# Optimization experiments

Hardware: AMD Instinct MI355X
Metric: run time of the kernel (lower is better)

Reference implementation:

```python
import jax, jax.numpy as jnp
import numpy as np

GROUPS = 32
EPS = 1e-5


def group_norm(x, gamma, beta):
    # x: [B, C, H, W]; normalize over (C//G, H, W) within each of G groups
    B, C, H, W = x.shape
    xg = x.reshape(B, GROUPS, C // GROUPS, H, W)
    mean = xg.mean(axis=(2, 3, 4), keepdims=True)
    var = xg.var(axis=(2, 3, 4), keepdims=True)
    xg = (xg - mean) * jax.lax.rsqrt(var + EPS)
    x = xg.reshape(B, C, H, W)
    return x * gamma[None, :, None, None] + beta[None, :, None, None]


def conv1x1(x, W, b):
    # 1x1 conv == pointwise linear over channels. x: [B,C,H,W], W: [Cout,Cin]
    return jnp.einsum('oc,bchw->bohw', W, x) + b[None, :, None, None]


def setup_inputs() -> dict:
    key = jax.random.key(0)
    ks = jax.random.split(key, 6)
    B, C, H, W = 16, 512, 32, 32
    scale = 1.0 / np.sqrt(C)  # ~kaiming-ish init for 1x1 convs
    return {
        'x': jax.random.normal(ks[0], (B, C, H, W), jnp.float32),
        'gn_gamma': jnp.ones((C,), jnp.float32),
        'gn_beta': jnp.zeros((C,), jnp.float32),
        'Wq': jax.random.normal(ks[1], (C, C), jnp.float32) * scale,
        'bq': jnp.zeros((C,), jnp.float32),
        'Wk': jax.random.normal(ks[2], (C, C), jnp.float32) * scale,
        'bk': jnp.zeros((C,), jnp.float32),
        'Wv': jax.random.normal(ks[3], (C, C), jnp.float32) * scale,
        'bv': jnp.zeros((C,), jnp.float32),
        'Wp': jax.random.normal(ks[4], (C, C), jnp.float32) * scale,
        'bp': jnp.zeros((C,), jnp.float32),
    }


def reference(x, gn_gamma, gn_beta, Wq, bq, Wk, bk, Wv, bv, Wp, bp):
    B, C, H, W = x.shape
    h = group_norm(x, gn_gamma, gn_beta)
    q = conv1x1(h, Wq, bq).reshape(B, C, H * W)  # [B,C,T]
    k = conv1x1(h, Wk, bk).reshape(B, C, H * W)
    v = conv1x1(h, Wv, bv).reshape(B, C, H * W)
    # scores [B, T(query), S(key)] = q^T k, scaled by C^{-1/2}
    w = jnp.einsum('bct,bcs->bts', q, k) * (C ** -0.5)
    w = jax.nn.softmax(w, axis=-1)
    h = jnp.einsum('bts,bcs->bct', w, v).reshape(B, C, H, W)
    h = conv1x1(h, Wp, bp)
    return x + h
```

## Files before the change

kernel.cpp:

```cpp
#include <hip/hip_runtime.h>

typedef unsigned short u16;
typedef __bf16 bf16x8 __attribute__((ext_vector_type(8)));
typedef float f32x4 __attribute__((ext_vector_type(4)));

__device__ __forceinline__ u16 f2bf(float f) {
    unsigned u = __builtin_bit_cast(unsigned, f);
    u += 0x7fffu + ((u >> 16) & 1u);
    return (u16)(u >> 16);
}
__device__ __forceinline__ float bf2f(u16 h) {
    return __builtin_bit_cast(float, (unsigned)h << 16);
}

#define GLDS16(g, l) __builtin_amdgcn_global_load_lds( \
    (const __attribute__((address_space(1))) void*)(g), \
    (__attribute__((address_space(3))) void*)(l), 16, 0, 0)

#define QK_SCALE 0.044194173824159216f

__global__ __launch_bounds__(256) void fused_pre(
    const float* __restrict__ Wq, const float* __restrict__ Wk,
    const float* __restrict__ Wv, const float* __restrict__ Wp,
    const float* __restrict__ bq, const float* __restrict__ bk,
    const float* __restrict__ bv,
    u16* __restrict__ Wqkv, u16* __restrict__ Wpb, float* __restrict__ bqkv,
    float* __restrict__ rsum,
    const float* __restrict__ x, float2* __restrict__ stats)
{
    __shared__ float rs[4], rs2[4];
    const int tid = threadIdx.x;

    if (blockIdx.x < 4096) {
        int idx = blockIdx.x * 256 + tid;
        if (idx < 786432) {
            int which = idx >> 18;
            int off   = idx & 262143;
            if (which == 0)
                Wqkv[idx] = f2bf(Wq[off] * QK_SCALE);
            else
                Wqkv[idx] = f2bf(((which == 1) ? Wk : Wv)[off]);
        } else {
            int off = idx - 786432;
            Wpb[off] = f2bf(Wp[off]);
        }
        if (idx < 1536) {
            float bvv = (idx < 512) ? bq[idx] * QK_SCALE
                      : (idx < 1024) ? bk[idx & 511] : bv[idx & 511];
            bqkv[idx] = bvv;
        }
        if (idx < 16384) rsum[idx] = 0.f;
        return;
    }

    const int rem = blockIdx.x - 4096;
    const int g = rem & 31, b = rem >> 5;
    const float* xg = x + ((size_t)b * 512 + (size_t)g * 16) * 1024;

    float s = 0.f, s2 = 0.f;
    const float4* x4 = (const float4*)xg;
    #pragma unroll 4
    for (int i = tid; i < 4096; i += 256) {
        float4 v = x4[i];
        s  += v.x + v.y + v.z + v.w;
        s2 += v.x * v.x + v.y * v.y + v.z * v.z + v.w * v.w;
    }
    #pragma unroll
    for (int off = 32; off; off >>= 1) {
        s  += __shfl_down(s, off);
        s2 += __shfl_down(s2, off);
    }
    const int w = tid >> 6;
    if ((tid & 63) == 0) { rs[w] = s; rs2[w] = s2; }
    __syncthreads();
    if (tid == 0) {
        float S  = rs[0] + rs[1] + rs[2] + rs[3];
        float S2 = rs2[0] + rs2[1] + rs2[2] + rs2[3];
        float mean = S * (1.f / 16384.f);
        float var  = S2 * (1.f / 16384.f) - mean * mean;
        stats[b * 32 + g] = make_float2(mean, rsqrtf(var + 1e-5f));
    }
}

__global__ __launch_bounds__(256) void gn_apply(
    const float* __restrict__ x, const float* __restrict__ gamma,
    const float* __restrict__ beta, const float2* __restrict__ stats,
    u16* __restrict__ ht)
{
    const int tc = blockIdx.x, b = blockIdx.y, tid = threadIdx.x;
    const int t0 = tc * 32;

    __shared__ float2 st[32];
    __shared__ float ga[512], be[512];
    __shared__ __align__(16) u16 tile[512 * 32];

    if (tid < 32) st[tid] = stats[b * 32 + tid];
    for (int c = tid; c < 512; c += 256) { ga[c] = gamma[c]; be[c] = beta[c]; }
    __syncthreads();

    #pragma unroll
    for (int pass = 0; pass < 16; pass++) {
        const int c = pass * 32 + (tid >> 3);
        const int f = tid & 7;
        float4 v = *(const float4*)(x + ((size_t)(b * 512 + c)) * 1024 + t0 + f * 4);
        float2 s = st[c >> 4];
        float sc = s.y * ga[c];
        float sh = be[c] - s.x * sc;
        ushort4 hv = {f2bf(v.x * sc + sh), f2bf(v.y * sc + sh),
                      f2bf(v.z * sc + sh), f2bf(v.w * sc + sh)};
        const int slot = f ^ (c & 7) ^ ((c >> 3) & 7);
        *(ushort4*)(tile + c * 32 + slot * 4) = hv;
    }
    __syncthreads();

    #pragma unroll
    for (int p = 0; p < 8; p++) {
        const int t = p * 4 + (tid >> 6);
        const int l = tid & 63;
        u16 tmp[8];
        #pragma unroll
        for (int e = 0; e < 8; e++) {
            const int c = l * 8 + e;
            const int slot = (t >> 2) ^ (c & 7) ^ ((c >> 3) & 7);
            tmp[e] = tile[c * 32 + slot * 4 + (t & 3)];
        }
        *(uint4*)(ht + ((size_t)b * 1024 + t0 + t) * 512 + l * 8) = *(uint4*)tmp;
    }
}

template <int MODE>
__global__ __launch_bounds__(512, 2) void gemm_big(
    const u16* __restrict__ A, const u16* __restrict__ B,
    size_t strideA, size_t strideB, int lda, int ldb, int K,
    u16* __restrict__ o0, u16* __restrict__ o1, u16* __restrict__ o2,
    const float* __restrict__ bias)
{
    __shared__ __align__(16) u16 smem[73728];
    u16* As = smem;
    u16* Bs = smem + 49152;

    const int tid  = threadIdx.x;
    const int lane = tid & 63;
    const int wave = tid >> 6;
    const int wm   = (wave & 3) * 64;
    const int wn   = (wave >> 2) * 64;

    const int gx = gridDim.x, gy = gridDim.y;
    int f = blockIdx.x + gx * (blockIdx.y + gy * blockIdx.z);
    const int nwg = gx * gy * (int)gridDim.z;
    f = (f & 7) * (nwg >> 3) + (f >> 3);
    const int bx  = f % gx;
    const int byz = f / gx;
    const int by  = byz % gy;
    const int b   = byz / gy;

    const u16* Ab = A + (size_t)b * strideA + (size_t)by * 256 * lda;
    const u16* Bb = B + (size_t)b * strideB + (size_t)bx * 128 * ldb;

    const int srow = tid >> 3;
    const int sc   = tid & 7;
    const int scg  = sc ^ (srow & 7);

    const u16* aSrc[4]; int aDst[4];
    #pragma unroll
    for (int u = 0; u < 4; u++) {
        aSrc[u] = Ab + (size_t)(u * 64 + srow) * lda + scg * 8;
        aDst[u] = (u * 64 + srow) * 64 + sc * 8;
    }
    const u16* bSrc[2]; int bDst[2];
    #pragma unroll
    for (int u = 0; u < 2; u++) {
        bSrc[u] = Bb + (size_t)(u * 64 + srow) * ldb + scg * 8;
        bDst[u] = (u * 64 + srow) * 64 + sc * 8;
    }

    const int l15 = lane & 15, lh = lane >> 4, rx = lane & 7;
    int aOff[4][2], bOff[4][2];
    #pragma unroll
    for (int i = 0; i < 4; i++)
        #pragma unroll
        for (int ks = 0; ks < 2; ks++) {
            const int slot = ((ks << 2) + lh) ^ rx;
            aOff[i][ks] = (wm + i * 16 + l15) * 64 + slot * 8;
            bOff[i][ks] = (wn + i * 16 + l15) * 64 + slot * 8;
        }

    f32x4 acc[4][4] = {};
    const int NT = K >> 6;

    #pragma unroll
    for (int u = 0; u < 4; u++) GLDS16(aSrc[u], As + aDst[u]);
    #pragma unroll
    for (int u = 0; u < 2; u++) GLDS16(bSrc[u], Bs + bDst[u]);
    #pragma unroll
    for (int u = 0; u < 4; u++) GLDS16(aSrc[u] + 64, As + 16384 + aDst[u]);
    #pragma unroll
    for (int u = 0; u < 2; u++) GLDS16(bSrc[u] + 64, Bs + 8192 + bDst[u]);

    int cbuf = 0, sbuf = 2;
    for (int t = 0; t < NT; ++t) {
        if (t == NT - 1) asm volatile("s_waitcnt vmcnt(0)" ::: "memory");
        else             asm volatile("s_waitcnt vmcnt(6)" ::: "memory");
        __builtin_amdgcn_s_barrier();

        const u16* Ac = As + cbuf * 16384;
        const u16* Bc = Bs + cbuf * 8192;
        u16* Asb = As + sbuf * 16384;
        u16* Bsb = Bs + sbuf * 8192;
        const int ko = (t + 2) * 64;
        const bool pf = (t + 2 < NT);

        if (pf) {
            GLDS16(aSrc[0] + ko, Asb + aDst[0]);
            GLDS16(aSrc[1] + ko, Asb + aDst[1]);
            GLDS16(bSrc[0] + ko, Bsb + bDst[0]);
        }
        {
            bf16x8 af[4], bfr[4];
            #pragma unroll
            for (int i = 0; i < 4; i++) {
                af[i]  = *(const bf16x8*)(Ac + aOff[i][0]);
                bfr[i] = *(const bf16x8*)(Bc + bOff[i][0]);
            }
            __builtin_amdgcn_s_setprio(1);
            #pragma unroll
            for (int mi = 0; mi < 4; mi++)
                #pragma unroll
                for (int nj = 0; nj < 4; nj++)
                    acc[mi][nj] = __builtin_amdgcn_mfma_f32_16x16x32_bf16(
                        af[mi], bfr[nj], acc[mi][nj], 0, 0, 0);
            __builtin_amdgcn_s_setprio(0);
        }
        if (pf) {
            GLDS16(aSrc[2] + ko, Asb + aDst[2]);
            GLDS16(aSrc[3] + ko, Asb + aDst[3]);
            GLDS16(bSrc[1] + ko, Bsb + bDst[1]);
        }
        {
            bf16x8 af[4], bfr[4];
            #pragma unroll
            for (int i = 0; i < 4; i++) {
                af[i]  = *(const bf16x8*)(Ac + aOff[i][1]);
                bfr[i] = *(const bf16x8*)(Bc + bOff[i][1]);
            }
            __builtin_amdgcn_s_setprio(1);
            #pragma unroll
            for (int mi = 0; mi < 4; mi++)
                #pragma unroll
                for (int nj = 0; nj < 4; nj++)
                    acc[mi][nj] = __builtin_amdgcn_mfma_f32_16x16x32_bf16(
                        af[mi], bfr[nj], acc[mi][nj], 0, 0, 0);
            __builtin_amdgcn_s_setprio(0);
        }

        cbuf = (cbuf == 2) ? 0 : cbuf + 1;
        sbuf = (sbuf == 2) ? 0 : sbuf + 1;
    }

    const int N0 = bx * 128;
    const int M0 = by * 256;

    if (N0 < 1024) {
        u16* dst = (N0 < 512) ? o0 : o1;
        const int nn0 = N0 & 511;
        #pragma unroll
        for (int nj = 0; nj < 4; nj++) {
            const int n = wn + nj * 16 + l15;
            const float bv = bias[N0 + n];
            #pragma unroll
            for (int mi = 0; mi < 4; mi++) {
                const int mq = M0 + wm + mi * 16 + lh * 4;
                const size_t base = ((size_t)b * 1024 + mq) * 512 + nn0 + n;
                dst[base]        = f2bf(acc[mi][nj][0] + bv);
                dst[base + 512]  = f2bf(acc[mi][nj][1] + bv);
                dst[base + 1024] = f2bf(acc[mi][nj][2] + bv);
                dst[base + 1536] = f2bf(acc[mi][nj][3] + bv);
            }
        }
    } else {
        __syncthreads();
        #pragma unroll
        for (int mi = 0; mi < 4; mi++) {
            const int mq = wm + mi * 16 + lh * 4;
            #pragma unroll
            for (int nj = 0; nj < 4; nj++) {
                const int n = wn + nj * 16 + l15;
                const float bv = bias[N0 + n];
                ushort4 hv = {f2bf(acc[mi][nj][0] + bv), f2bf(acc[mi][nj][1] + bv),
                              f2bf(acc[mi][nj][2] + bv), f2bf(acc[mi][nj][3] + bv)};
                *(ushort4*)((char*)smem + n * 512 +
                            (((mq >> 3) ^ (n & 31)) << 4) + ((mq >> 2) & 1) * 8) = hv;
            }
        }
        __syncthreads();
        #pragma unroll
        for (int p = 0; p < 8; p++) {
            const int n  = p * 16 + (tid >> 5);
            const int gi = tid & 31;
            uint4 v4 = *(const uint4*)((char*)smem + n * 512 +
                                       ((gi ^ (n & 31)) << 4));
            u16* dst = o2 + ((size_t)b * 512 + (N0 - 1024) + n) * 1024 + M0;
            *(uint4*)(dst + gi * 8) = v4;
        }
    }
}

template <int MODE>
__global__ __launch_bounds__(256, 4) void gemm128(
    const u16* __restrict__ A, const u16* __restrict__ B,
    size_t strideA, size_t strideB, int lda, int ldb, int K,
    u16* __restrict__ o0,
    float* __restrict__ fo, const float* __restrict__ bias,
    const float* __restrict__ xres)
{
    __shared__ __align__(16) u16 sm[16384];
    u16* As = sm;
    u16* Bs = sm + 8192;

    const int tid  = threadIdx.x;
    const int lane = tid & 63;
    const int wave = tid >> 6;
    const int wm   = (wave >> 1) * 64;
    const int wn   = (wave & 1) * 64;
    const int l15  = lane & 15;
    const int lh   = lane >> 4;
    const int rx   = lane & 7;

    const int gx = gridDim.x, gy = gridDim.y;
    int f = blockIdx.x + gx * (blockIdx.y + gy * blockIdx.z);
    const int nwg = gx * gy * (int)gridDim.z;
    f = (f & 7) * (nwg >> 3) + (f >> 3);
    const int bx  = f % gx;
    const int byz = f / gx;
    const int by  = byz % gy;
    const int b   = byz / gy;

    const u16* Ab = A + (size_t)b * strideA + (size_t)by * 128 * lda;
    const u16* Bb = B + (size_t)b * strideB + (size_t)bx * 128 * ldb;

    const int srow = lane >> 3;
    const int sc   = lane & 7;
    const int scg  = sc ^ srow;

    int aOff[4][2], bOff[4][2];
    #pragma unroll
    for (int i = 0; i < 4; i++)
        #pragma unroll
        for (int ks = 0; ks < 2; ks++) {
            const int slot = ((ks << 2) + lh) ^ rx;
            aOff[i][ks] = (wm + i * 16 + l15) * 64 + slot * 8;
            bOff[i][ks] = (wn + i * 16 + l15) * 64 + slot * 8;
        }

    f32x4 acc[4][4] = {};

    for (int k0 = 0; k0 < K; k0 += 64) {
        __syncthreads();
        #pragma unroll
        for (int s = 0; s < 4; s++) {
            const int r = wave * 32 + s * 8 + srow;
            GLDS16(Ab + (size_t)r * lda + k0 + scg * 8, As + r * 64 + sc * 8);
            GLDS16(Bb + (size_t)r * ldb + k0 + scg * 8, Bs + r * 64 + sc * 8);
        }
        __syncthreads();

        #pragma unroll
        for (int ks = 0; ks < 2; ks++) {
            bf16x8 af[4], bfr[4];
            #pragma unroll
            for (int i = 0; i < 4; i++) {
                af[i]  = *(const bf16x8*)(As + aOff[i][ks]);
                bfr[i] = *(const bf16x8*)(Bs + bOff[i][ks]);
            }
            __builtin_amdgcn_s_setprio(1);
            #pragma unroll
            for (int mi = 0; mi < 4; mi++)
                #pragma unroll
                for (int nj = 0; nj < 4; nj++)
                    acc[mi][nj] = __builtin_amdgcn_mfma_f32_16x16x32_bf16(
                        af[mi], bfr[nj], acc[mi][nj], 0, 0, 0);
            __builtin_amdgcn_s_setprio(0);
        }
    }

    const int N0 = bx * 128;
    const int M0 = by * 128;

    if (MODE != 3) {
        __syncthreads();
        float rinv_[4];
        if (MODE == 2) {
            #pragma unroll
            for (int nj = 0; nj < 4; nj++)
                rinv_[nj] = 1.0f / xres[(size_t)b * 1024 + N0 + wn + nj * 16 + l15];
        }
        #pragma unroll
        for (int mi = 0; mi < 4; mi++) {
            const int mq  = wm + mi * 16 + lh * 4;
            const int gsl = mq >> 3;
            const int gb  = ((mq >> 2) & 1) * 8;
            #pragma unroll
            for (int nj = 0; nj < 4; nj++) {
                const int n = wn + nj * 16 + l15;
                float a0 = acc[mi][nj][0], a1 = acc[mi][nj][1];
                float a2 = acc[mi][nj][2], a3 = acc[mi][nj][3];
                if (MODE == 1) {
                    a0 = __expf(a0); a1 = __expf(a1);
                    a2 = __expf(a2); a3 = __expf(a3);
                }
                if (MODE == 2) {
                    a0 *= rinv_[nj]; a1 *= rinv_[nj];
                    a2 *= rinv_[nj]; a3 *= rinv_[nj];
                }
                ushort4 hv = {f2bf(a0), f2bf(a1), f2bf(a2), f2bf(a3)};
                *(ushort4*)((char*)sm + n * 256 +
                            ((gsl ^ (n & 15)) << 4) + gb) = hv;
            }
        }
        __syncthreads();
        #pragma unroll
        for (int p = 0; p < 8; p++) {
            const int n  = p * 16 + (tid >> 4);
            const int gi = tid & 15;
            uint4 v = *(const uint4*)((char*)sm + n * 256 + ((gi ^ (n & 15)) << 4));
            u16* dst;
            if (MODE == 1) dst = o0 + ((size_t)b * 1024 + N0 + n) * 1024 + M0;
            else           dst = o0 + ((size_t)b * 1024 + N0 + n) * 512 + M0;
            *(uint4*)(dst + gi * 8) = v;
            if (MODE == 1) {
                unsigned wd_[4] = {v.x, v.y, v.z, v.w};
                float rsm = 0.f;
                #pragma unroll
                for (int q = 0; q < 4; q++)
                    rsm += __builtin_bit_cast(float, wd_[q] << 16)
                         + __builtin_bit_cast(float, wd_[q] & 0xffff0000u);
                #pragma unroll
                for (int off = 1; off < 16; off <<= 1)
                    rsm += __shfl_xor(rsm, off);
                if (gi == 0)
                    atomicAdd(fo + ((size_t)b * 1024 + N0 + n), rsm);
            }
        }
    } else {
        float* smf = (float*)sm;
        #pragma unroll
        for (int half = 0; half < 2; half++) {
            __syncthreads();
            if ((wave >> 1) == half) {
                #pragma unroll
                for (int mi = 0; mi < 4; mi++) {
                    const int mloc = mi * 16 + lh * 4;
                    const int gsl  = mloc >> 2;
                    #pragma unroll
                    for (int nj = 0; nj < 4; nj++) {
                        const int n = wn + nj * 16 + l15;
                        float4 v4 = {acc[mi][nj][0], acc[mi][nj][1],
                                     acc[mi][nj][2], acc[mi][nj][3]};
                        *(float4*)((char*)smf + n * 256 +
                                   ((gsl ^ (n & 15)) << 4)) = v4;
                    }
                }
            }
            __syncthreads();
            #pragma unroll
            for (int p = 0; p < 8; p++) {
                const int n  = p * 16 + (tid >> 4);
                const int gi = tid & 15;
                float4 v = *(const float4*)((char*)smf + n * 256 +
                                            ((gi ^ (n & 15)) << 4));
                const int m = half * 64 + gi * 4;
                const size_t off = ((size_t)b * 512 + N0 + n) * 1024 + M0 + m;
                const float bv = bias[N0 + n];
                const float4 xv = *(const float4*)(xres + off);
                float4 ov = {v.x + bv + xv.x, v.y + bv + xv.y,
                             v.z + bv + xv.z, v.w + bv + xv.w};
                *(float4*)(fo + off) = ov;
            }
        }
    }
}

extern "C" void kernel_launch(void* const* d_in, const int* in_sizes, int n_in,
                              void* d_out, int out_size, void* d_ws, size_t ws_size,
                              hipStream_t stream)
{
    const float* x     = (const float*)d_in[0];
    const float* gamma = (const float*)d_in[1];
    const float* beta  = (const float*)d_in[2];
    const float* Wq    = (const float*)d_in[3];
    const float* bq    = (const float*)d_in[4];
    const float* Wk    = (const float*)d_in[5];
    const float* bk    = (const float*)d_in[6];
    const float* Wv    = (const float*)d_in[7];
    const float* bv    = (const float*)d_in[8];
    const float* Wp    = (const float*)d_in[9];
    const float* bp    = (const float*)d_in[10];

    char* ws = (char*)d_ws;
    u16*   Wqkv   = (u16*)(ws + 0);
    u16*   Wpb    = (u16*)(ws + 1572864);
    float* bqkv   = (float*)(ws + 2097152);
    u16*   ht     = (u16*)(ws + 2105344);
    u16*   kt     = (u16*)(ws + 18882560);
    u16*   vv     = (u16*)(ws + 35659776);
    u16*   scores = (u16*)(ws + 52436992);
    u16*   qt  = (u16*)d_out;
    float2* stats = (float2*)((char*)d_out + 16777216);
    float* rsum   = (float*)((char*)d_out + 16781312);
    u16*   h2  = ht;
    float* out = (float*)d_out;

    fused_pre<<<4608, 256, 0, stream>>>(Wq, Wk, Wv, Wp, bq, bk, bv,
                                        Wqkv, Wpb, bqkv, rsum, x, stats);
    gn_apply<<<dim3(32, 16), 256, 0, stream>>>(x, gamma, beta, stats, ht);

    gemm_big<0><<<dim3(12, 4, 16), 512, 0, stream>>>(
        ht, Wqkv, 524288, 0, 512, 512, 512,
        qt, kt, vv, bqkv);

    gemm128<1><<<dim3(8, 8, 16), 256, 0, stream>>>(
        kt, qt, 524288, 524288, 512, 512, 512,
        scores, rsum, nullptr, nullptr);

    gemm128<2><<<dim3(8, 4, 16), 256, 0, stream>>>(
        vv, scores, 524288, 1048576, 1024, 1024, 1024,
        h2, nullptr, nullptr, rsum);

    gemm128<3><<<dim3(4, 8, 16), 256, 0, stream>>>(
        h2, Wpb, 524288, 0, 512, 512, 512,
        nullptr, out, bp, x);
}
```

Before: 221.4 us.

## Fuse GroupNorm stats and apply into one kernel; run scores GEMM on big tile kernel

Merges the weight-conversion/stats kernel and the GroupNorm apply kernel into one launch. Each block keeps its group's 16x1024 slice in LDS, computes the statistics, and writes the normalized transposed bf16 output directly, which removes a second read of x and one kernel launch. Weight conversion is also vectorized to eight elements per thread. The QK^T scores GEMM moves from the 128-tile kernel to the 256x128 gemm_big kernel, with a new exp, transpose and row-sum epilogue. The single-group blocks use 64KB of LDS, and the store pattern of 32-byte chunks at a 1KB stride may coalesce poorly.

```diff
diff --git a/kernel.cpp b/kernel.cpp
--- a/kernel.cpp
+++ b/kernel.cpp
@@ -19,49 +19,52 @@
 
 #define QK_SCALE 0.044194173824159216f
 
-__global__ __launch_bounds__(256) void fused_pre(
+__global__ __launch_bounds__(256) void gn_fused(
     const float* __restrict__ Wq, const float* __restrict__ Wk,
     const float* __restrict__ Wv, const float* __restrict__ Wp,
     const float* __restrict__ bq, const float* __restrict__ bk,
     const float* __restrict__ bv,
+    const float* __restrict__ x, const float* __restrict__ gamma,
+    const float* __restrict__ beta,
     u16* __restrict__ Wqkv, u16* __restrict__ Wpb, float* __restrict__ bqkv,
-    float* __restrict__ rsum,
-    const float* __restrict__ x, float2* __restrict__ stats)
+    float* __restrict__ rsum, u16* __restrict__ ht)
 {
-    __shared__ float rs[4], rs2[4];
-    const int tid = threadIdx.x;
-
-    if (blockIdx.x < 4096) {
-        int idx = blockIdx.x * 256 + tid;
-        if (idx < 786432) {
-            int which = idx >> 18;
-            int off   = idx & 262143;
-            if (which == 0)
-                Wqkv[idx] = f2bf(Wq[off] * QK_SCALE);
-            else
-                Wqkv[idx] = f2bf(((which == 1) ? Wk : Wv)[off]);
-        } else {
-            int off = idx - 786432;
-            Wpb[off] = f2bf(Wp[off]);
-        }
-        if (idx < 1536) {
-            float bvv = (idx < 512) ? bq[idx] * QK_SCALE
-                      : (idx < 1024) ? bk[idx & 511] : bv[idx & 511];
-            bqkv[idx] = bvv;
-        }
-        if (idx < 16384) rsum[idx] = 0.f;
-        return;
-    }
-
-    const int rem = blockIdx.x - 4096;
-    const int g = rem & 31, b = rem >> 5;
-    const float* xg = x + ((size_t)b * 512 + (size_t)g * 16) * 1024;
-
+    __shared__ float xs[16 * 1024];
+    __shared__ float rs[4], rs2[4], stat2[2];
+
+    const int tid  = threadIdx.x;
+    const int blk  = blockIdx.x;
+    const int gidx = blk * 256 + tid;
+
+    {
+        const int base  = gidx * 8;
+        const int which = base >> 18;
+        const int off   = base & 262143;
+        const float* src = (which == 0) ? Wq + off
+                         : (which == 1) ? Wk + off
+                         : (which == 2) ? Wv + off : Wp + off;
+        const float sc = (which == 0) ? QK_SCALE : 1.0f;
+        float4 a = ((const float4*)src)[0];
+        float4 c = ((const float4*)src)[1];
+        u16 h[8] = {f2bf(a.x * sc), f2bf(a.y * sc), f2bf(a.z * sc), f2bf(a.w * sc),
+                    f2bf(c.x * sc), f2bf(c.y * sc), f2bf(c.z * sc), f2bf(c.w * sc)};
+        if (which < 3) *(uint4*)(Wqkv + base) = *(uint4*)h;
+        else           *(uint4*)(Wpb + (base - 786432)) = *(uint4*)h;
+    }
+    if (gidx < 1536) {
+        bqkv[gidx] = (gidx < 512) ? bq[gidx] * QK_SCALE
+                   : (gidx < 1024) ? bk[gidx & 511] : bv[gidx & 511];
+    }
+    if (gidx < 16384) rsum[gidx] = 0.f;
+
+    const int b = blk >> 5, g = blk & 31;
+    const float4* xg4 = (const float4*)(x + ((size_t)b * 512 + (size_t)g * 16) * 1024);
+    float4* xs4 = (float4*)xs;
     float s = 0.f, s2 = 0.f;
-    const float4* x4 = (const float4*)xg;
-    #pragma unroll 4
-    for (int i = tid; i < 4096; i += 256) {
-        float4 v = x4[i];
+    #pragma unroll
+    for (int i = 0; i < 16; i++) {
+        float4 v = xg4[i * 256 + tid];
+        xs4[i * 256 + tid] = v;
         s  += v.x + v.y + v.z + v.w;
         s2 += v.x * v.x + v.y * v.y + v.z * v.z + v.w * v.w;
     }
@@ -78,53 +81,30 @@
         float S2 = rs2[0] + rs2[1] + rs2[2] + rs2[3];
         float mean = S * (1.f / 16384.f);
         float var  = S2 * (1.f / 16384.f) - mean * mean;
-        stats[b * 32 + g] = make_float2(mean, rsqrtf(var + 1e-5f));
-    }
-}
-
-__global__ __launch_bounds__(256) void gn_apply(
-    const float* __restrict__ x, const float* __restrict__ gamma,
-    const float* __restrict__ beta, const float2* __restrict__ stats,
-    u16* __restrict__ ht)
-{
-    const int tc = blockIdx.x, b = blockIdx.y, tid = threadIdx.x;
-    const int t0 = tc * 32;
-
-    __shared__ float2 st[32];
-    __shared__ float ga[512], be[512];
-    __shared__ __align__(16) u16 tile[512 * 32];
-
-    if (tid < 32) st[tid] = stats[b * 32 + tid];
-    for (int c = tid; c < 512; c += 256) { ga[c] = gamma[c]; be[c] = beta[c]; }
+        stat2[0] = mean;
+        stat2[1] = rsqrtf(var + 1e-5f);
+    }
     __syncthreads();
-
-    #pragma unroll
-    for (int pass = 0; pass < 16; pass++) {
-        const int c = pass * 32 + (tid >> 3);
-        const int f = tid & 7;
-        float4 v = *(const float4*)(x + ((size_t)(b * 512 + c)) * 1024 + t0 + f * 4);
-        float2 s = st[c >> 4];
-        float sc = s.y * ga[c];
-        float sh = be[c] - s.x * sc;
-        ushort4 hv = {f2bf(v.x * sc + sh), f2bf(v.y * sc + sh),
-                      f2bf(v.z * sc + sh), f2bf(v.w * sc + sh)};
-        const int slot = f ^ (c & 7) ^ ((c >> 3) & 7);
-        *(ushort4*)(tile + c * 32 + slot * 4) = hv;
-    }
-    __syncthreads();
-
-    #pragma unroll
-    for (int p = 0; p < 8; p++) {
-        const int t = p * 4 + (tid >> 6);
-        const int l = tid & 63;
-        u16 tmp[8];
-        #pragma unroll
-        for (int e = 0; e < 8; e++) {
-            const int c = l * 8 + e;
-            const int slot = (t >> 2) ^ (c & 7) ^ ((c >> 3) & 7);
-            tmp[e] = tile[c * 32 + slot * 4 + (t & 3)];
-        }
-        *(uint4*)(ht + ((size_t)b * 1024 + t0 + t) * 512 + l * 8) = *(uint4*)tmp;
+    const float mean = stat2[0], rstd = stat2[1];
+
+    float scl[16], shf[16];
+    #pragma unroll
+    for (int c = 0; c < 16; c++) {
+        float ga = gamma[g * 16 + c];
+        scl[c] = rstd * ga;
+        shf[c] = beta[g * 16 + c] - mean * scl[c];
+    }
+
+    #pragma unroll
+    for (int i = 0; i < 4; i++) {
+        const int t = i * 256 + tid;
+        u16 h[16];
+        #pragma unroll
+        for (int c = 0; c < 16; c++)
+            h[c] = f2bf(xs[c * 1024 + t] * scl[c] + shf[c]);
+        uint4* d = (uint4*)(ht + ((size_t)b * 1024 + t) * 512 + g * 16);
+        d[0] = ((uint4*)h)[0];
+        d[1] = ((uint4*)h)[1];
     }
 }
 
@@ -133,7 +113,7 @@
     const u16* __restrict__ A, const u16* __restrict__ B,
     size_t strideA, size_t strideB, int lda, int ldb, int K,
     u16* __restrict__ o0, u16* __restrict__ o1, u16* __restrict__ o2,
-    const float* __restrict__ bias)
+    float* __restrict__ fo, const float* __restrict__ bias)
 {
     __shared__ __align__(16) u16 smem[73728];
     u16* As = smem;
@@ -260,7 +240,44 @@
     const int N0 = bx * 128;
     const int M0 = by * 256;
 
-    if (N0 < 1024) {
+    if (MODE == 1) {
+        __syncthreads();
+        #pragma unroll
+        for (int mi = 0; mi < 4; mi++) {
+            const int mq = wm + mi * 16 + lh * 4;
+            #pragma unroll
+            for (int nj = 0; nj < 4; nj++) {
+                const int n = wn + nj * 16 + l15;
+                ushort4 hv = {f2bf(__expf(acc[mi][nj][0])),
+                              f2bf(__expf(acc[mi][nj][1])),
+                              f2bf(__expf(acc[mi][nj][2])),
+                              f2bf(__expf(acc[mi][nj][3]))};
+                *(ushort4*)((char*)smem + n * 512 +
+                            (((mq >> 3) ^ (n & 31)) << 4) + ((mq >> 2) & 1) * 8) = hv;
+            }
+        }
+        __syncthreads();
+        #pragma unroll
+        for (int p = 0; p < 8; p++) {
+            const int n  = p * 16 + (tid >> 5);
+            const int gi = tid & 31;
+            uint4 v4 = *(const uint4*)((char*)smem + n * 512 +
+                                       ((gi ^ (n & 31)) << 4));
+            u16* dst = o0 + ((size_t)b * 1024 + N0 + n) * 1024 + M0;
+            *(uint4*)(dst + gi * 8) = v4;
+            unsigned wd_[4] = {v4.x, v4.y, v4.z, v4.w};
+            float rsm = 0.f;
+            #pragma unroll
+            for (int q = 0; q < 4; q++)
+                rsm += __builtin_bit_cast(float, wd_[q] << 16)
+                     + __builtin_bit_cast(float, wd_[q] & 0xffff0000u);
+            #pragma unroll
+            for (int off = 1; off < 32; off <<= 1)
+                rsm += __shfl_xor(rsm, off);
+            if (gi == 0)
+                atomicAdd(fo + ((size_t)b * 1024 + N0 + n), rsm);
+        }
+    } else if (N0 < 1024) {
         u16* dst = (N0 < 512) ? o0 : o1;
         const int nn0 = N0 & 511;
         #pragma unroll
@@ -404,10 +421,6 @@
                 const int n = wn + nj * 16 + l15;
                 float a0 = acc[mi][nj][0], a1 = acc[mi][nj][1];
                 float a2 = acc[mi][nj][2], a3 = acc[mi][nj][3];
-                if (MODE == 1) {
-                    a0 = __expf(a0); a1 = __expf(a1);
-                    a2 = __expf(a2); a3 = __expf(a3);
-                }
                 if (MODE == 2) {
                     a0 *= rinv_[nj]; a1 *= rinv_[nj];
                     a2 *= rinv_[nj]; a3 *= rinv_[nj];
@@ -423,23 +436,8 @@
             const int n  = p * 16 + (tid >> 4);
             const int gi = tid & 15;
             uint4 v = *(const uint4*)((char*)sm + n * 256 + ((gi ^ (n & 15)) << 4));
-            u16* dst;
-            if (MODE == 1) dst = o0 + ((size_t)b * 1024 + N0 + n) * 1024 + M0;
-            else           dst = o0 + ((size_t)b * 1024 + N0 + n) * 512 + M0;
+            u16* dst = o0 + ((size_t)b * 1024 + N0 + n) * 512 + M0;
             *(uint4*)(dst + gi * 8) = v;
-            if (MODE == 1) {
-                unsigned wd_[4] = {v.x, v.y, v.z, v.w};
-                float rsm = 0.f;
-                #pragma unroll
-                for (int q = 0; q < 4; q++)
-                    rsm += __builtin_bit_cast(float, wd_[q] << 16)
-                         + __builtin_bit_cast(float, wd_[q] & 0xffff0000u);
-                #pragma unroll
-                for (int off = 1; off < 16; off <<= 1)
-                    rsm += __shfl_xor(rsm, off);
-                if (gi == 0)
-                    atomicAdd(fo + ((size_t)b * 1024 + N0 + n), rsm);
-            }
         }
     } else {
         float* smf = (float*)sm;
@@ -505,22 +503,21 @@
     u16*   vv     = (u16*)(ws + 35659776);
     u16*   scores = (u16*)(ws + 52436992);
     u16*   qt  = (u16*)d_out;
-    float2* stats = (float2*)((char*)d_out + 16777216);
     float* rsum   = (float*)((char*)d_out + 16781312);
     u16*   h2  = ht;
     float* out = (float*)d_out;
 
-    fused_pre<<<4608, 256, 0, stream>>>(Wq, Wk, Wv, Wp, bq, bk, bv,
-                                        Wqkv, Wpb, bqkv, rsum, x, stats);
-    gn_apply<<<dim3(32, 16), 256, 0, stream>>>(x, gamma, beta, stats, ht);
+    gn_fused<<<512, 256, 0, stream>>>(Wq, Wk, Wv, Wp, bq, bk, bv,
+                                      x, gamma, beta,
+                                      Wqkv, Wpb, bqkv, rsum, ht);
 
     gemm_big<0><<<dim3(12, 4, 16), 512, 0, stream>>>(
         ht, Wqkv, 524288, 0, 512, 512, 512,
-        qt, kt, vv, bqkv);
-
-    gemm128<1><<<dim3(8, 8, 16), 256, 0, stream>>>(
+        qt, kt, vv, nullptr, bqkv);
+
+    gemm_big<1><<<dim3(8, 4, 16), 512, 0, stream>>>(
         kt, qt, 524288, 524288, 512, 512, 512,
-        scores, rsum, nullptr, nullptr);
+        scores, nullptr, nullptr, rsum, nullptr);
 
     gemm128<2><<<dim3(8, 4, 16), 256, 0, stream>>>(
         vv, scores, 524288, 1048576, 1024, 1024, 1024,
```

Result: faster. 208.8 us (median of 2 runs) (-5.7%).
